# Optimization experiments

Hardware: AMD Instinct MI355X
Metric: run time of the kernel (lower is better)

The kernel has to match this reference:

```python
import jax, jax.numpy as jnp
import numpy as np

B, T, E, H = 4, 2048, 1024, 16
S = E // H  # 64


def setup_inputs() -> dict:
    key = jax.random.key(0)
    ks = jax.random.split(key, 6)
    return {
        "x": jax.random.normal(ks[0], (B, T, E), dtype=jnp.float32),
        "Wk": jax.random.normal(ks[1], (S, S), dtype=jnp.float32) * (1.0 / np.sqrt(S)),
        "Wq": jax.random.normal(ks[2], (S, S), dtype=jnp.float32) * (1.0 / np.sqrt(S)),
        "Wv": jax.random.normal(ks[3], (S, S), dtype=jnp.float32) * (1.0 / np.sqrt(S)),
        "Wp": jax.random.normal(ks[4], (E, E), dtype=jnp.float32) * (1.0 / np.sqrt(E)),
        "bp": jnp.zeros((E,), dtype=jnp.float32),
    }


def reference(x, Wk, Wq, Wv, Wp, bp):
    b, t, e = x.shape
    h, s = H, S
    xh = x.reshape(b, t, h, s)
    # per-head projections share one (s,s) weight across all heads (torch Linear: y = x @ W.T)
    keys = jnp.einsum('bthi,oi->bhto', xh, Wk)     # (b,h,t,s)
    queries = jnp.einsum('bthi,oi->bhto', xh, Wq)
    values = jnp.einsum('bthi,oi->bhto', xh, Wv)
    scale = e ** 0.25  # q and k each divided by e^(1/4) -> net 1/sqrt(e)
    queries = queries / scale
    keys = keys / scale
    dot = jnp.einsum('bhqs,bhks->bhqk', queries, keys)  # (b,h,t,t)
    attn = jax.nn.softmax(dot, axis=-1)
    out = jnp.einsum('bhqk,bhks->bqhs', attn, values)   # (b,t,h,s)
    out = out.reshape(b, t, h * s)
    return jnp.einsum('bte,oe->bto', out, Wp) + bp
```

## Files before the change

kernel.cpp:

```cpp
#include <hip/hip_runtime.h>
#include <hip/hip_bf16.h>

#define Bv 4
#define Tv 2048
#define Ev 1024
#define Hv 16
#define Sv 64

typedef __attribute__((ext_vector_type(8))) short bf16x8;
typedef __attribute__((ext_vector_type(4))) float f32x4;
typedef __attribute__((ext_vector_type(16))) float f32x16;

__device__ __forceinline__ ushort f2bf(float f) {
    unsigned u = __float_as_uint(f);
    u = (u + 0x7FFFu + ((u >> 16) & 1u)) >> 16;
    return (ushort)u;
}
__device__ __forceinline__ unsigned pkrn(float a, float b) {
    __hip_bfloat162 t = __float22bfloat162_rn(make_float2(a, b));
    unsigned r; __builtin_memcpy(&r, &t, 4); return r;
}
__device__ __forceinline__ unsigned pktr(float a, float b) {
    return __builtin_amdgcn_perm(__float_as_uint(b), __float_as_uint(a), 0x07060302u);
}

__device__ __forceinline__ void async16(void* lds, const void* g) {
    __builtin_amdgcn_global_load_lds(
        (const __attribute__((address_space(1))) unsigned int*)g,
        (__attribute__((address_space(3))) unsigned int*)lds, 16, 0, 0);
}

__global__ __launch_bounds__(192) void qkv_kernel(
    const float* __restrict__ x,
    const float* __restrict__ Wq, const float* __restrict__ Wk,
    const float* __restrict__ Wv, const float* __restrict__ Wp,
    ushort* __restrict__ Wpb,
    ushort* __restrict__ Q, ushort* __restrict__ K, ushort* __restrict__ Vt)
{
    if (blockIdx.x >= 2048) {
        size_t i = ((size_t)(blockIdx.x - 2048) * 192 + threadIdx.x) * 8;
        if (i < (size_t)Ev * Ev) {
            float4 v0 = *(const float4*)(Wp + i);
            float4 v1 = *(const float4*)(Wp + i + 4);
            uint4 o = {pkrn(v0.x, v0.y), pkrn(v0.z, v0.w),
                       pkrn(v1.x, v1.y), pkrn(v1.z, v1.w)};
            *(uint4*)(Wpb + i) = o;
        }
        return;
    }

    __shared__ float xs[16 * 256];

    const int tid  = threadIdx.x;
    const int wave = tid >> 6;
    const int lane = tid & 63;
    const int m    = lane & 15;
    const int quad = lane >> 4;

    const int tt = blockIdx.x >> 2;
    const int hg = blockIdx.x & 3;
    const int g0 = tt * 16;
    const int b  = g0 >> 11;
    const int t0 = g0 & 2047;

    #pragma unroll
    for (int pass = 0; pass < 6; ++pass) {
        int c = pass * 192 + tid;
        if (c < 1024) {
            int tok  = c >> 6;
            int gsrc = (c & 63) ^ (tok & 7);
            async16(&xs[c * 4],
                    x + (size_t)(g0 + tok) * Ev + hg * 256 + gsrc * 4);
        }
    }

    const float* Wsel = (wave == 0) ? Wq : ((wave == 1) ? Wk : Wv);
    const float wscale = (wave == 0) ? 0.03125f * 1.4426950408889634f : 1.0f;
    bf16x8 wf[4][2];
    #pragma unroll
    for (int ot = 0; ot < 4; ++ot)
        #pragma unroll
        for (int ks = 0; ks < 2; ++ks) {
            const float* ws = &Wsel[(ot * 16 + m) * 64 + ks * 32 + quad * 8];
            float4 w0 = *(const float4*)ws;
            float4 w1 = *(const float4*)(ws + 4);
            unsigned pk[4];
            pk[0] = pkrn(w0.x * wscale, w0.y * wscale);
            pk[1] = pkrn(w0.z * wscale, w0.w * wscale);
            pk[2] = pkrn(w1.x * wscale, w1.y * wscale);
            pk[3] = pkrn(w1.z * wscale, w1.w * wscale);
            wf[ot][ks] = *(bf16x8*)pk;
        }

    __syncthreads();

    #pragma unroll
    for (int hi = 0; hi < 4; ++hi) {
        const int h  = hg * 4 + hi;
        const int bh = b * Hv + h;

        bf16x8 xf[2];
        #pragma unroll
        for (int ks = 0; ks < 2; ++ks) {
            int gc = hi * 16 + ks * 8 + quad * 2;
            float4 v0 = *(const float4*)&xs[(m * 64 + ( gc      ^ (m & 7))) * 4];
            float4 v1 = *(const float4*)&xs[(m * 64 + ((gc + 1) ^ (m & 7))) * 4];
            unsigned pk[4];
            pk[0] = pkrn(v0.x, v0.y); pk[1] = pkrn(v0.z, v0.w);
            pk[2] = pkrn(v1.x, v1.y); pk[3] = pkrn(v1.z, v1.w);
            xf[ks] = *(bf16x8*)pk;
        }

        f32x4 acc[4];
        #pragma unroll
        for (int ot = 0; ot < 4; ++ot) acc[ot] = (f32x4){0.f, 0.f, 0.f, 0.f};

        if (wave < 2) {
            #pragma unroll
            for (int ks = 0; ks < 2; ++ks)
                #pragma unroll
                for (int ot = 0; ot < 4; ++ot)
                    acc[ot] = __builtin_amdgcn_mfma_f32_16x16x32_bf16(
                        xf[ks], wf[ot][ks], acc[ot], 0, 0, 0);
            ushort* dst = ((wave == 0) ? Q : K) + ((size_t)bh * Tv + t0) * Sv;
            #pragma unroll
            for (int ot = 0; ot < 4; ++ot)
                #pragma unroll
                for (int r = 0; r < 4; ++r)
                    dst[(quad * 4 + r) * Sv + ot * 16 + m]
                        = (ushort)pkrn(acc[ot][r], acc[ot][r]);
        } else {
            #pragma unroll
            for (int ks = 0; ks < 2; ++ks)
                #pragma unroll
                for (int st = 0; st < 4; ++st)
                    acc[st] = __builtin_amdgcn_mfma_f32_16x16x32_bf16(
                        xf[ks], wf[st][ks], acc[st], 0, 0, 0);
            ushort* vr = Vt + ((size_t)bh * Sv + m) * Tv + t0 + quad * 4;
            #pragma unroll
            for (int st = 0; st < 4; ++st) {
                uint2 w = {pkrn(acc[st][0], acc[st][1]), pkrn(acc[st][2], acc[st][3])};
                *(uint2*)(vr + (size_t)st * 16 * Tv) = w;
            }
        }
    }
}

__global__ __launch_bounds__(256, 2) void attn_kernel(
    const ushort* __restrict__ Q, const ushort* __restrict__ K,
    const ushort* __restrict__ Vt, ushort* __restrict__ O)
{
    __shared__ ushort kl[2][64 * 64];
    __shared__ ushort vl[2][64 * 64];
    __shared__ float  ll[4][64];

    const int tid  = threadIdx.x;
    const int wave = tid >> 6;
    const int lane = tid & 63;
    const int r31  = lane & 31;
    const int hi   = lane >> 5;
    const int bh   = blockIdx.x & 63;
    const int q0   = (blockIdx.x >> 6) << 8;

    const ushort* Qb = Q + ((size_t)bh * Tv + q0 + wave * 64 + r31) * Sv + hi * 8;
    bf16x8 qf[2][4];
    #pragma unroll
    for (int g = 0; g < 2; ++g)
        #pragma unroll
        for (int ks = 0; ks < 4; ++ks)
            qf[g][ks] = *(const bf16x8*)(Qb + (size_t)g * 32 * Sv + ks * 16);

    f32x16 oa[2][2];
    #pragma unroll
    for (int g = 0; g < 2; ++g)
        #pragma unroll
        for (int st = 0; st < 2; ++st)
            #pragma unroll
            for (int r = 0; r < 16; ++r)
                oa[g][st][r] = 0.f;
    float lsum[2] = {0.f, 0.f};

    const ushort* Kb = K  + (size_t)bh * Tv * Sv;
    const ushort* Vb = Vt + (size_t)bh * Sv * Tv;

    const int r0 = tid >> 3,         cg0 = (tid & 7) ^ (r0 & 7);
    const int r1 = (256 + tid) >> 3, cg1 = ((256 + tid) & 7) ^ (r1 & 7);
    const size_t koff0 = (size_t)r0 * Sv + cg0 * 8;
    const size_t koff1 = (size_t)r1 * Sv + cg1 * 8;
    const size_t voff0 = (size_t)r0 * Tv + cg0 * 8;
    const size_t voff1 = (size_t)r1 * Tv + cg1 * 8;
    const int swz = r31 & 7;

    auto softpv = [&](const f32x16& sv, float& ls, f32x16* oag, int kp,
                      const bf16x8* vf) {
        float p[8];
        #pragma unroll
        for (int j = 0; j < 8; ++j)
            p[j] = __builtin_amdgcn_exp2f(sv[kp * 8 + j]);
        ls += ((p[0] + p[1]) + (p[2] + p[3]))
            + ((p[4] + p[5]) + (p[6] + p[7]));
        unsigned d0 = pktr(p[0], p[1]);
        unsigned d1 = pktr(p[2], p[3]);
        unsigned d2 = pktr(p[4], p[5]);
        unsigned d3 = pktr(p[6], p[7]);
        asm volatile("v_permlane32_swap_b32 %0, %1" : "+v"(d0), "+v"(d2));
        asm volatile("v_permlane32_swap_b32 %0, %1" : "+v"(d1), "+v"(d3));
        unsigned pw[4] = {d0, d1, d2, d3};
        bf16x8 pf = *(bf16x8*)pw;
        #pragma unroll
        for (int st = 0; st < 2; ++st)
            oag[st] = __builtin_amdgcn_mfma_f32_32x32x16_bf16(
                pf, vf[st], oag[st], 0, 0, 0);
    };

    uint4 rk0 = *(const uint4*)(Kb + koff0);
    uint4 rk1 = *(const uint4*)(Kb + koff1);
    uint4 rv0 = *(const uint4*)(Vb + voff0);
    uint4 rv1 = *(const uint4*)(Vb + voff1);
    *(uint4*)&kl[0][(size_t)tid * 8]         = rk0;
    *(uint4*)&kl[0][((size_t)tid + 256) * 8] = rk1;
    *(uint4*)&vl[0][(size_t)tid * 8]         = rv0;
    *(uint4*)&vl[0][((size_t)tid + 256) * 8] = rv1;
    rk0 = *(const uint4*)(Kb + (size_t)64 * Sv + koff0);
    rk1 = *(const uint4*)(Kb + (size_t)64 * Sv + koff1);
    rv0 = *(const uint4*)(Vb + 64 + voff0);
    rv1 = *(const uint4*)(Vb + 64 + voff1);
    __syncthreads();

    for (int k0 = 0; k0 < Tv; k0 += 64) {
        const int cur = (k0 >> 6) & 1;

        *(uint4*)&kl[cur ^ 1][(size_t)tid * 8]         = rk0;
        *(uint4*)&kl[cur ^ 1][((size_t)tid + 256) * 8] = rk1;
        *(uint4*)&vl[cur ^ 1][(size_t)tid * 8]         = rv0;
        *(uint4*)&vl[cur ^ 1][((size_t)tid + 256) * 8] = rv1;

        int kn = k0 + 128; if (kn >= Tv) kn = 0;
        rk0 = *(const uint4*)(Kb + (size_t)kn * Sv + koff0);
        rk1 = *(const uint4*)(Kb + (size_t)kn * Sv + koff1);
        rv0 = *(const uint4*)(Vb + kn + voff0);
        rv1 = *(const uint4*)(Vb + kn + voff1);

        #pragma unroll
        for (int kt = 0; kt < 2; ++kt) {
            bf16x8 kf[4];
            #pragma unroll
            for (int ks = 0; ks < 4; ++ks)
                kf[ks] = *(const bf16x8*)
                    &kl[cur][(kt * 32 + r31) * 64 + (((ks * 2 + hi) ^ swz) * 8)];

            f32x16 s0, s1;
            #pragma unroll
            for (int r = 0; r < 16; ++r) { s0[r] = 0.f; s1[r] = 0.f; }
            #pragma unroll
            for (int ks = 0; ks < 4; ++ks)
                s0 = __builtin_amdgcn_mfma_f32_32x32x16_bf16(
                    kf[ks], qf[0][ks], s0, 0, 0, 0);
            #pragma unroll
            for (int ks = 0; ks < 4; ++ks)
                s1 = __builtin_amdgcn_mfma_f32_32x32x16_bf16(
                    kf[ks], qf[1][ks], s1, 0, 0, 0);

            #pragma unroll
            for (int kp = 0; kp < 2; ++kp) {
                const int kc = (kt * 2 + kp) * 2 + hi;
                bf16x8 vf[2];
                #pragma unroll
                for (int st = 0; st < 2; ++st)
                    vf[st] = *(const bf16x8*)
                        &vl[cur][(st * 32 + r31) * 64 + ((kc ^ swz) * 8)];
                softpv(s0, lsum[0], oa[0], kp, vf);
                softpv(s1, lsum[1], oa[1], kp, vf);
            }
        }

        __syncthreads();
    }

    lsum[0] += __shfl_xor(lsum[0], 32, 64);
    lsum[1] += __shfl_xor(lsum[1], 32, 64);
    if (hi == 0) {
        ll[wave][r31]      = 1.0f / lsum[0];
        ll[wave][32 + r31] = 1.0f / lsum[1];
    }

    const int b = bh >> 4, h = bh & 15;
    #pragma unroll
    for (int g = 0; g < 2; ++g) {
        float sc[16];
        #pragma unroll
        for (int r = 0; r < 16; ++r)
            sc[r] = ll[wave][g * 32 + (r & 3) + 4 * hi + 8 * (r >> 2)];
        #pragma unroll
        for (int st = 0; st < 2; ++st)
            #pragma unroll
            for (int r = 0; r < 16; ++r) {
                const int q = (r & 3) + 4 * hi + 8 * (r >> 2);
                O[((size_t)(b * Tv + q0 + wave * 64 + g * 32 + q)) * Ev
                  + h * Sv + st * 32 + r31] = f2bf(oa[g][st][r] * sc[r]);
            }
    }
}

__global__ __launch_bounds__(256) void proj_kernel(
    const ushort* __restrict__ A, const ushort* __restrict__ Bw,
    const float* __restrict__ bp, float* __restrict__ C)
{
    __shared__ ushort Asm[2][128 * 32];
    __shared__ ushort Bsm[2][128 * 32];
    const int tid  = threadIdx.x;
    const int wave = tid >> 6;
    const int lane = tid & 63;
    const int m    = lane & 15;
    const int quad = lane >> 4;
    const int wm   = wave >> 1;
    const int wn   = wave & 1;
    const int m0   = blockIdx.x * 128;
    const int n0   = blockIdx.y * 128;

    f32x4 acc[4][4];
    #pragma unroll
    for (int i = 0; i < 4; ++i)
        #pragma unroll
        for (int j = 0; j < 4; ++j)
            acc[i][j] = (f32x4){0.f, 0.f, 0.f, 0.f};

    const int row0 = tid >> 2,         col0 = (tid & 3) * 8;
    const int row1 = (256 + tid) >> 2, col1 = ((256 + tid) & 3) * 8;

    uint4 a0 = *(const uint4*)&A [(size_t)(m0 + row0) * Ev + col0];
    uint4 a1 = *(const uint4*)&A [(size_t)(m0 + row1) * Ev + col1];
    uint4 b0 = *(const uint4*)&Bw[(size_t)(n0 + row0) * Ev + col0];
    uint4 b1 = *(const uint4*)&Bw[(size_t)(n0 + row1) * Ev + col1];
    *(uint4*)&Asm[0][(size_t)tid * 8]         = a0;
    *(uint4*)&Asm[0][((size_t)tid + 256) * 8] = a1;
    *(uint4*)&Bsm[0][(size_t)tid * 8]         = b0;
    *(uint4*)&Bsm[0][((size_t)tid + 256) * 8] = b1;
    a0 = *(const uint4*)&A [(size_t)(m0 + row0) * Ev + 32 + col0];
    a1 = *(const uint4*)&A [(size_t)(m0 + row1) * Ev + 32 + col1];
    b0 = *(const uint4*)&Bw[(size_t)(n0 + row0) * Ev + 32 + col0];
    b1 = *(const uint4*)&Bw[(size_t)(n0 + row1) * Ev + 32 + col1];
    __syncthreads();

    for (int it = 0; it < 32; ++it) {
        const int cur = it & 1;
        if (it < 31) {
            *(uint4*)&Asm[cur ^ 1][(size_t)tid * 8]         = a0;
            *(uint4*)&Asm[cur ^ 1][((size_t)tid + 256) * 8] = a1;
            *(uint4*)&Bsm[cur ^ 1][(size_t)tid * 8]         = b0;
            *(uint4*)&Bsm[cur ^ 1][((size_t)tid + 256) * 8] = b1;
            int kn = (it + 2) * 32; if (kn >= Ev) kn = 0;
            a0 = *(const uint4*)&A [(size_t)(m0 + row0) * Ev + kn + col0];
            a1 = *(const uint4*)&A [(size_t)(m0 + row1) * Ev + kn + col1];
            b0 = *(const uint4*)&Bw[(size_t)(n0 + row0) * Ev + kn + col0];
            b1 = *(const uint4*)&Bw[(size_t)(n0 + row1) * Ev + kn + col1];
        }

        bf16x8 af[4], bf[4];
        #pragma unroll
        for (int i = 0; i < 4; ++i)
            af[i] = *(const bf16x8*)&Asm[cur][(wm * 64 + i * 16 + m) * 32 + quad * 8];
        #pragma unroll
        for (int j = 0; j < 4; ++j)
            bf[j] = *(const bf16x8*)&Bsm[cur][(wn * 64 + j * 16 + m) * 32 + quad * 8];
        #pragma unroll
        for (int i = 0; i < 4; ++i)
            #pragma unroll
            for (int j = 0; j < 4; ++j)
                acc[i][j] = __builtin_amdgcn_mfma_f32_16x16x32_bf16(
                    af[i], bf[j], acc[i][j], 0, 0, 0);

        __syncthreads();
    }

    float bbv[4];
    #pragma unroll
    for (int j = 0; j < 4; ++j)
        bbv[j] = bp[n0 + wn * 64 + j * 16 + m];

    #pragma unroll
    for (int i = 0; i < 4; ++i)
        #pragma unroll
        for (int j = 0; j < 4; ++j)
            #pragma unroll
            for (int r = 0; r < 4; ++r)
                C[(size_t)(m0 + wm * 64 + i * 16 + quad * 4 + r) * Ev
                  + n0 + wn * 64 + j * 16 + m] = acc[i][j][r] + bbv[j];
}

extern "C" void kernel_launch(void* const* d_in, const int* in_sizes, int n_in,
                              void* d_out, int out_size, void* d_ws, size_t ws_size,
                              hipStream_t stream) {
    const float* x  = (const float*)d_in[0];
    const float* Wk = (const float*)d_in[1];
    const float* Wq = (const float*)d_in[2];
    const float* Wv = (const float*)d_in[3];
    const float* Wp = (const float*)d_in[4];
    const float* bp = (const float*)d_in[5];
    float* out = (float*)d_out;

    ushort* Q   = (ushort*)d_ws;
    ushort* K   = Q   + 8388608;
    ushort* Vt  = K   + 8388608;
    ushort* O   = Vt  + 8388608;
    ushort* Wpb = O   + 8388608;

    qkv_kernel<<<2731, 192, 0, stream>>>(x, Wq, Wk, Wv, Wp, Wpb, Q, K, Vt);
    attn_kernel<<<512, 256, 0, stream>>>(Q, K, Vt, O);
    proj_kernel<<<dim3(64, 8), 256, 0, stream>>>(O, Wpb, bp, out);
}
```

Measured before the change: 205.8 us.

## Replace register-staged K/V prefetch with async global-to-LDS triple buffering

The K and V tiles are now loaded with async16 direct global-to-LDS copies into a three-slot ring, two tiles ahead, instead of going through registers into a double buffer. This drops the uint4 staging registers and the explicit LDS stores, which should ease VGPR pressure and cut instruction issue in the main loop. In exchange, LDS use per block grows by half, and correctness depends on __syncthreads draining the outstanding async copies before each slot is read.

```diff
diff --git a/kernel.cpp b/kernel.cpp
--- a/kernel.cpp
+++ b/kernel.cpp
@@ -150,8 +150,8 @@
     const ushort* __restrict__ Q, const ushort* __restrict__ K,
     const ushort* __restrict__ Vt, ushort* __restrict__ O)
 {
-    __shared__ ushort kl[2][64 * 64];
-    __shared__ ushort vl[2][64 * 64];
+    __shared__ ushort kl[3][64 * 64];
+    __shared__ ushort vl[3][64 * 64];
     __shared__ float  ll[4][64];
 
     const int tid  = threadIdx.x;
@@ -213,33 +213,21 @@
                 pf, vf[st], oag[st], 0, 0, 0);
     };
 
-    uint4 rk0 = *(const uint4*)(Kb + koff0);
-    uint4 rk1 = *(const uint4*)(Kb + koff1);
-    uint4 rv0 = *(const uint4*)(Vb + voff0);
-    uint4 rv1 = *(const uint4*)(Vb + voff1);
-    *(uint4*)&kl[0][(size_t)tid * 8]         = rk0;
-    *(uint4*)&kl[0][((size_t)tid + 256) * 8] = rk1;
-    *(uint4*)&vl[0][(size_t)tid * 8]         = rv0;
-    *(uint4*)&vl[0][((size_t)tid + 256) * 8] = rv1;
-    rk0 = *(const uint4*)(Kb + (size_t)64 * Sv + koff0);
-    rk1 = *(const uint4*)(Kb + (size_t)64 * Sv + koff1);
-    rv0 = *(const uint4*)(Vb + 64 + voff0);
-    rv1 = *(const uint4*)(Vb + 64 + voff1);
+    auto stage = [&](int t, int s) {
+        const size_t kk = (size_t)t * 64;
+        async16(&kl[s][(size_t)tid * 8],         Kb + kk * Sv + koff0);
+        async16(&kl[s][((size_t)tid + 256) * 8], Kb + kk * Sv + koff1);
+        async16(&vl[s][(size_t)tid * 8],         Vb + kk + voff0);
+        async16(&vl[s][((size_t)tid + 256) * 8], Vb + kk + voff1);
+    };
+
+    stage(0, 0);
+    stage(1, 1);
     __syncthreads();
 
-    for (int k0 = 0; k0 < Tv; k0 += 64) {
-        const int cur = (k0 >> 6) & 1;
-
-        *(uint4*)&kl[cur ^ 1][(size_t)tid * 8]         = rk0;
-        *(uint4*)&kl[cur ^ 1][((size_t)tid + 256) * 8] = rk1;
-        *(uint4*)&vl[cur ^ 1][(size_t)tid * 8]         = rv0;
-        *(uint4*)&vl[cur ^ 1][((size_t)tid + 256) * 8] = rv1;
-
-        int kn = k0 + 128; if (kn >= Tv) kn = 0;
-        rk0 = *(const uint4*)(Kb + (size_t)kn * Sv + koff0);
-        rk1 = *(const uint4*)(Kb + (size_t)kn * Sv + koff1);
-        rv0 = *(const uint4*)(Vb + kn + voff0);
-        rv1 = *(const uint4*)(Vb + kn + voff1);
+    int cur = 0;
+    for (int t = 0; t < 32; ++t) {
+        if (t < 30) stage(t + 2, (cur == 0) ? 2 : cur - 1);
 
         #pragma unroll
         for (int kt = 0; kt < 2; ++kt) {
@@ -275,6 +263,7 @@
         }
 
         __syncthreads();
+        cur = (cur == 2) ? 0 : cur + 1;
     }
 
     lsum[0] += __shfl_xor(lsum[0], 32, 64);
```

Result: no change. 209.7 us (+1.9%).
